# Kernel optimization log

Hardware: AMD Instinct MI355X
Metric: run time of the kernel (lower is better)

Reference implementation:

```python
import jax, jax.numpy as jnp
import numpy as np

N_NODES = 100000
N_EDGES = 1600000
D_IN = 128
D_OUT = 128


def setup_inputs() -> dict:
    key = jax.random.key(0)
    k1, k2, k3 = jax.random.split(key, 3)
    x = jax.random.normal(k1, (N_NODES, D_IN), dtype=jnp.float32)
    edge_index = jax.random.randint(k2, (2, N_EDGES), 0, N_NODES, dtype=jnp.int64)
    # glorot-style init for the lazily-created weight
    scale = jnp.sqrt(6.0 / (D_IN + D_OUT)).astype(jnp.float32)
    weight = jax.random.uniform(k3, (D_IN, D_OUT), dtype=jnp.float32, minval=-1.0, maxval=1.0) * scale
    bias = jnp.zeros((D_OUT,), dtype=jnp.float32)
    return {"x": x, "edge_index": edge_index, "weight": weight, "bias": bias}


def reference(x, edge_index, weight, bias):
    N = x.shape[0]
    row, col = edge_index[0], edge_index[1]
    # add_remaining_self_loops: drop existing self-loops (equivalently zero their
    # weight) and append a self-loop of weight 1.0 for every node (improved=False).
    ew = jnp.where(row == col, 0.0, 1.0).astype(x.dtype)
    loop = jnp.arange(N, dtype=row.dtype)
    row = jnp.concatenate([row, loop])
    col = jnp.concatenate([col, loop])
    ew = jnp.concatenate([ew, jnp.ones((N,), dtype=x.dtype)])
    # degree via scatter-add on destination (col), deg^{-1/2} with inf -> 0
    deg = jax.ops.segment_sum(ew, col, num_segments=N)
    deg_inv_sqrt = jnp.where(deg > 0, jax.lax.rsqrt(deg), 0.0).astype(x.dtype)
    norm = deg_inv_sqrt[row] * ew * deg_inv_sqrt[col]  # [E+N]
    # dense transform then gather-scale-scatter (GCN message passing, aggr='add')
    xw = x @ weight  # [N, D_OUT]
    msgs = norm[:, None] * xw[row]  # [E+N, D_OUT] gather on source nodes
    out = jax.ops.segment_sum(msgs, col, num_segments=N)  # scatter-add to dest
    return out + bias
```

## Files before the change

### kernel.cpp

```cpp
#include <hip/hip_runtime.h>
#include <hip/hip_bf16.h>

#define NN 100000
#define NE 1600000
#define D  128
#define NPAD 100352
#define NBLK 782
#define CAP  64

#define BSH    9
#define NB_C   196
#define CAPB   9216
#define PCHUNK 2048
#define PEPT   8
#define NPART  782

#define NSL    8
#define NGRP   3125
#define AGG_BLOCKS 2048

typedef __attribute__((ext_vector_type(8))) short short8;
typedef __attribute__((ext_vector_type(4))) float floatx4;
typedef __attribute__((ext_vector_type(2))) float fx2;
typedef __attribute__((ext_vector_type(4))) int intx4;

__device__ __forceinline__ unsigned short f2b(float f) {
    __hip_bfloat16 h = __float2bfloat16(f);
    return *(unsigned short*)&h;
}

__device__ __forceinline__ int swz(int row, int col_us) {
    return row * 128 + (col_us ^ ((row & 7) << 3));
}

__global__ __launch_bounds__(256) void k_part(const int* __restrict__ row,
                                              const int* __restrict__ col,
                                              int* __restrict__ bcnt,
                                              unsigned int* __restrict__ edgesP) {
    __shared__ int cur[NB_C], basep[NB_C];
    int t = threadIdx.x;
    size_t e0 = (size_t)blockIdx.x * PCHUNK;

    for (int i = t; i < NB_C; i += 256) cur[i] = 0;
    __syncthreads();

    unsigned int val[PEPT];
    int bk[PEPT], rk[PEPT];
#pragma unroll
    for (int i = 0; i < PEPT; ++i) {
        size_t e = e0 + i * 256 + t;
        bk[i] = -1;
        if (e < NE) {
            int r = row[e], c = col[e];
            if (r != c) {
                bk[i]  = c >> BSH;
                val[i] = (unsigned)r | ((unsigned)(c & 511) << 17);
                rk[i]  = atomicAdd(&cur[bk[i]], 1);
            }
        }
    }
    __syncthreads();

    for (int i = t; i < NB_C; i += 256)
        basep[i] = cur[i] ? atomicAdd(&bcnt[i], cur[i]) : 0;
    __syncthreads();

#pragma unroll
    for (int i = 0; i < PEPT; ++i) {
        if (bk[i] >= 0) {
            int pos = basep[bk[i]] + rk[i];
            if (pos < CAPB) edgesP[(size_t)bk[i] * CAPB + pos] = val[i];
        }
    }
}

__global__ __launch_bounds__(1024) void k_fine(const int* __restrict__ bcnt,
                                               const unsigned int* __restrict__ edgesP,
                                               int* __restrict__ counts,
                                               float* __restrict__ dinv,
                                               int* __restrict__ srcs) {
    __shared__ int cnt[512];
    int t = threadIdx.x, b = blockIdx.x;
    int n0 = b << BSH;
    for (int i = t; i < 512; i += 1024) cnt[i] = 0;
    __syncthreads();

    int m = min(bcnt[b], CAPB);
    const unsigned int* ep = edgesP + (size_t)b * CAPB;
    for (int i = t; i < m; i += 1024) {
        unsigned int v = ep[i];
        int c0 = v >> 17;
        int s  = v & 0x1FFFF;
        int pos = atomicAdd(&cnt[c0], 1);
        if (pos < CAP) srcs[(size_t)(n0 + c0) * CAP + pos] = s;
    }
    __syncthreads();
    for (int i = t; i < 512; i += 1024) {
        int n = n0 + i;
        int cv = cnt[i];
        counts[n] = min(cv, CAP);
        dinv[n] = rsqrtf((float)cv + 1.0f);
    }
}

__global__ void k_prep_w(const float* __restrict__ w, unsigned short* __restrict__ wt) {
    int i = blockIdx.x * 256 + threadIdx.x;
    int n = i >> 7, k = i & 127;
    wt[swz(n, k)] = f2b(w[k * D + n]);
}

__global__ __launch_bounds__(256, 2) void k_gemm_mfma(const float* __restrict__ x,
                                                      const unsigned short* __restrict__ wt,
                                                      const float* __restrict__ dinv,
                                                      unsigned short* __restrict__ yw) {
    __shared__ unsigned short sX[128 * 128];
    __shared__ unsigned short sW[128 * 128];
    __shared__ float sD[128];
    int tid = threadIdx.x;
    long row0 = (long)blockIdx.x * 128;

    if (tid < 128) {
        long gr = row0 + tid;
        sD[tid] = (gr < NN) ? dinv[gr] : 0.0f;
    }
    {
        const uint4* src = (const uint4*)wt;
        uint4* dst = (uint4*)sW;
#pragma unroll
        for (int j = 0; j < 8; ++j) dst[tid + j * 256] = src[tid + j * 256];
    }
#pragma unroll
    for (int j = 0; j < 16; ++j) {
        int i = tid + j * 256;
        int r = i >> 5, q = i & 31;
        floatx4 v = {0.f, 0.f, 0.f, 0.f};
        long gr = row0 + r;
        if (gr < NN) v = __builtin_nontemporal_load((const floatx4*)(x + gr * D + q * 4));
        ushort4 u;
        u.x = f2b(v.x); u.y = f2b(v.y); u.z = f2b(v.z); u.w = f2b(v.w);
        *(ushort4*)&sX[swz(r, q * 4)] = u;
    }
    __syncthreads();

    int lane = tid & 63, wave = tid >> 6;
    int wm = (wave & 1) * 64, wn = (wave >> 1) * 64;
    int lrow = lane & 15, lkb = (lane >> 4) * 8;

    floatx4 acc[4][4] = {};
#pragma unroll
    for (int kc = 0; kc < 4; ++kc) {
        int kb = kc * 32 + lkb;
        short8 bfr[4];
#pragma unroll
        for (int tn = 0; tn < 4; ++tn)
            bfr[tn] = *(const short8*)&sW[swz(wn + tn * 16 + lrow, kb)];
#pragma unroll
        for (int tm = 0; tm < 4; ++tm) {
            short8 afr = *(const short8*)&sX[swz(wm + tm * 16 + lrow, kb)];
#pragma unroll
            for (int tn = 0; tn < 4; ++tn)
                acc[tm][tn] = __builtin_amdgcn_mfma_f32_16x16x32_bf16(afr, bfr[tn], acc[tm][tn], 0, 0, 0);
        }
    }

    int orow = (lane >> 4) * 4;
    int ocol = lane & 15;
    int wb = wn >> 4;
#pragma unroll
    for (int tm = 0; tm < 4; ++tm) {
#pragma unroll
        for (int reg = 0; reg < 4; ++reg) {
            int  rt = wm + tm * 16 + orow + reg;
            long m  = row0 + rt;
            if (m < NN) {
                float dm = sD[rt];
                unsigned short* o = yw + ((size_t)wb * NN + m) * 16 + ocol;
#pragma unroll
                for (int tn = 0; tn < 4; ++tn)
                    o[(size_t)tn * NN * 16] = f2b(acc[tm][tn][reg] * dm);
            }
        }
    }
}

__global__ __launch_bounds__(256, 8) void k_agg(const int* __restrict__ counts,
                                                const int* __restrict__ srcs,
                                                const float* __restrict__ dinv,
                                                const unsigned int* __restrict__ ywd,
                                                const float* __restrict__ bias,
                                                float* __restrict__ out) {
    __shared__ int slds[32 * 40];
    int tid = threadIdx.x;
    int w = tid >> 6;
    int d = (tid >> 3) & 7;
    int j = tid & 7;
    int din = w * 8 + d;
    int sl = blockIdx.x & 7;

    const unsigned int* ywj = ywd + (size_t)sl * NN * 8 + j;
    fx2 b2 = *(const fx2*)(bias + sl * 16 + 2 * j);

    int r = tid >> 3, q = tid & 7;

    for (int grp = blockIdx.x >> 3; grp < NGRP; grp += AGG_BLOCKS / 8) {
        int c0 = grp * 32;
        {
            intx4 v = __builtin_nontemporal_load(
                (const intx4*)(srcs + (size_t)(c0 + r) * CAP + q * 4));
            *(intx4*)&slds[r * 40 + q * 4] = v;
        }
        __syncthreads();

        int c = c0 + din;
        int cnt = counts[c];
        float dc = dinv[c];
        const int* srow = slds + din * 40;

        unsigned int v0 = ywj[(size_t)c * 8];
        float a0 = __uint_as_float(v0 << 16);
        float a1 = __uint_as_float(v0 & 0xFFFF0000u);

        int lim = min(cnt, 32);
        int p = 0;
        for (; p + 4 <= lim; p += 4) {
            intx4 s4 = *(const intx4*)(srow + p);
            unsigned int g0 = ywj[(size_t)s4.x * 8];
            unsigned int g1 = ywj[(size_t)s4.y * 8];
            unsigned int g2 = ywj[(size_t)s4.z * 8];
            unsigned int g3 = ywj[(size_t)s4.w * 8];
            a0 += __uint_as_float(g0 << 16);  a1 += __uint_as_float(g0 & 0xFFFF0000u);
            a0 += __uint_as_float(g1 << 16);  a1 += __uint_as_float(g1 & 0xFFFF0000u);
            a0 += __uint_as_float(g2 << 16);  a1 += __uint_as_float(g2 & 0xFFFF0000u);
            a0 += __uint_as_float(g3 << 16);  a1 += __uint_as_float(g3 & 0xFFFF0000u);
        }
        for (; p < lim; ++p) {
            unsigned int g = ywj[(size_t)srow[p] * 8];
            a0 += __uint_as_float(g << 16);  a1 += __uint_as_float(g & 0xFFFF0000u);
        }
        if (cnt > 32) {
            const int* sp2 = srcs + (size_t)c * CAP;
            for (p = 32; p < cnt; ++p) {
                unsigned int g = ywj[(size_t)sp2[p] * 8];
                a0 += __uint_as_float(g << 16);  a1 += __uint_as_float(g & 0xFFFF0000u);
            }
        }

        fx2 o;
        o.x = dc * a0 + b2.x;
        o.y = dc * a1 + b2.y;
        __builtin_nontemporal_store(o, (fx2*)(out + (size_t)c * D + sl * 16 + 2 * j));
        __syncthreads();
    }
}

extern "C" void kernel_launch(void* const* d_in, const int* in_sizes, int n_in,
                              void* d_out, int out_size, void* d_ws, size_t ws_size,
                              hipStream_t stream) {
    const float* x    = (const float*)d_in[0];
    const int*   ei   = (const int*)d_in[1];
    const float* w    = (const float*)d_in[2];
    const float* bias = (const float*)d_in[3];
    float*       out  = (float*)d_out;

    const int* row = ei;
    const int* col = ei + NE;

    int*   counts = (int*)d_ws;
    float* dinv   = (float*)(counts + NPAD);
    int*   srcs   = (int*)(dinv + NPAD);
    unsigned short* yw = (unsigned short*)(srcs + (size_t)NN * CAP);
    unsigned short* wt = yw + (size_t)NN * D;
    int*   bcnt   = (int*)(wt + 128 * 128);
    unsigned int* edgesP = (unsigned int*)yw;

    hipMemsetAsync(bcnt, 0, NB_C * sizeof(int), stream);

    k_prep_w<<<64, 256, 0, stream>>>(w, wt);
    k_part<<<NPART, 256, 0, stream>>>(row, col, bcnt, edgesP);
    k_fine<<<NB_C, 1024, 0, stream>>>(bcnt, edgesP, counts, dinv, srcs);
    k_gemm_mfma<<<NBLK, 256, 0, stream>>>(x, wt, dinv, yw);
    k_agg<<<AGG_BLOCKS, 256, 0, stream>>>(counts, srcs, dinv, (const unsigned int*)yw, bias, out);
}
```

Baseline: 260.1 us.

## Process one destination per wave with shuffle-broadcast gathers and coalesced GEMM stores

The aggregation kernel now assigns one destination node per wavefront. Eight lane groups each gather a different source row's 16-column slice, and the partial sums are combined with cross-lane xor shuffles. This replaces the older layout of 32 destinations per block with an LDS staging buffer and block-wide barriers. The GEMM epilogue now stages its bf16 results through shared memory so that each row slice is written as contiguous 32-byte vector stores instead of scattered 2-byte stores. The new aggregation caps neighbours at 63 per node, and it wastes lanes on low-degree nodes because each wave handles a single destination.

```diff
diff --git a/kernel.cpp b/kernel.cpp
--- a/kernel.cpp
+++ b/kernel.cpp
@@ -15,14 +15,12 @@
 #define PEPT   8
 #define NPART  782
 
-#define NSL    8
-#define NGRP   3125
 #define AGG_BLOCKS 2048
+#define DESTS_PER_ROUND 1024
 
 typedef __attribute__((ext_vector_type(8))) short short8;
 typedef __attribute__((ext_vector_type(4))) float floatx4;
 typedef __attribute__((ext_vector_type(2))) float fx2;
-typedef __attribute__((ext_vector_type(4))) int intx4;
 
 __device__ __forceinline__ unsigned short f2b(float f) {
     __hip_bfloat16 h = __float2bfloat16(f);
@@ -163,22 +161,34 @@
         }
     }
 
+    __syncthreads();
+
     int orow = (lane >> 4) * 4;
     int ocol = lane & 15;
-    int wb = wn >> 4;
 #pragma unroll
     for (int tm = 0; tm < 4; ++tm) {
 #pragma unroll
         for (int reg = 0; reg < 4; ++reg) {
-            int  rt = wm + tm * 16 + orow + reg;
-            long m  = row0 + rt;
-            if (m < NN) {
-                float dm = sD[rt];
-                unsigned short* o = yw + ((size_t)wb * NN + m) * 16 + ocol;
-#pragma unroll
-                for (int tn = 0; tn < 4; ++tn)
-                    o[(size_t)tn * NN * 16] = f2b(acc[tm][tn][reg] * dm);
-            }
+            int rt = wm + tm * 16 + orow + reg;
+            float dm = sD[rt];
+#pragma unroll
+            for (int tn = 0; tn < 4; ++tn)
+                sX[swz(rt, wn + tn * 16 + ocol)] = f2b(acc[tm][tn][reg] * dm);
+        }
+    }
+    __syncthreads();
+
+#pragma unroll
+    for (int j = 0; j < 4; ++j) {
+        int i = tid + j * 256;
+        int r = i & 127, sl8 = i >> 7;
+        long gr = row0 + r;
+        if (gr < NN) {
+            uint4 v0 = *(const uint4*)&sX[swz(r, sl8 * 16)];
+            uint4 v1 = *(const uint4*)&sX[swz(r, sl8 * 16 + 8)];
+            unsigned short* dst = yw + ((size_t)sl8 * NN + gr) * 16;
+            *(uint4*)dst = v0;
+            *(uint4*)(dst + 8) = v1;
         }
     }
 }
@@ -189,67 +199,49 @@
                                                 const unsigned int* __restrict__ ywd,
                                                 const float* __restrict__ bias,
                                                 float* __restrict__ out) {
-    __shared__ int slds[32 * 40];
-    int tid = threadIdx.x;
-    int w = tid >> 6;
-    int d = (tid >> 3) & 7;
-    int j = tid & 7;
-    int din = w * 8 + d;
+    int lane = threadIdx.x & 63;
+    int wv = threadIdx.x >> 6;
     int sl = blockIdx.x & 7;
-
-    const unsigned int* ywj = ywd + (size_t)sl * NN * 8 + j;
+    int g = lane >> 3, j = lane & 7;
+
+    const unsigned int* yws = ywd + (size_t)sl * NN * 8 + j;
     fx2 b2 = *(const fx2*)(bias + sl * 16 + 2 * j);
 
-    int r = tid >> 3, q = tid & 7;
-
-    for (int grp = blockIdx.x >> 3; grp < NGRP; grp += AGG_BLOCKS / 8) {
-        int c0 = grp * 32;
-        {
-            intx4 v = __builtin_nontemporal_load(
-                (const intx4*)(srcs + (size_t)(c0 + r) * CAP + q * 4));
-            *(intx4*)&slds[r * 40 + q * 4] = v;
-        }
-        __syncthreads();
-
-        int c = c0 + din;
-        int cnt = counts[c];
-        float dc = dinv[c];
-        const int* srow = slds + din * 40;
-
-        unsigned int v0 = ywj[(size_t)c * 8];
-        float a0 = __uint_as_float(v0 << 16);
-        float a1 = __uint_as_float(v0 & 0xFFFF0000u);
-
-        int lim = min(cnt, 32);
-        int p = 0;
-        for (; p + 4 <= lim; p += 4) {
-            intx4 s4 = *(const intx4*)(srow + p);
-            unsigned int g0 = ywj[(size_t)s4.x * 8];
-            unsigned int g1 = ywj[(size_t)s4.y * 8];
-            unsigned int g2 = ywj[(size_t)s4.z * 8];
-            unsigned int g3 = ywj[(size_t)s4.w * 8];
-            a0 += __uint_as_float(g0 << 16);  a1 += __uint_as_float(g0 & 0xFFFF0000u);
-            a0 += __uint_as_float(g1 << 16);  a1 += __uint_as_float(g1 & 0xFFFF0000u);
-            a0 += __uint_as_float(g2 << 16);  a1 += __uint_as_float(g2 & 0xFFFF0000u);
-            a0 += __uint_as_float(g3 << 16);  a1 += __uint_as_float(g3 & 0xFFFF0000u);
-        }
-        for (; p < lim; ++p) {
-            unsigned int g = ywj[(size_t)srow[p] * 8];
-            a0 += __uint_as_float(g << 16);  a1 += __uint_as_float(g & 0xFFFF0000u);
-        }
-        if (cnt > 32) {
-            const int* sp2 = srcs + (size_t)c * CAP;
-            for (p = 32; p < cnt; ++p) {
-                unsigned int g = ywj[(size_t)sp2[p] * 8];
-                a0 += __uint_as_float(g << 16);  a1 += __uint_as_float(g & 0xFFFF0000u);
+    for (int c = (blockIdx.x >> 3) * 4 + wv; c < NN; c += DESTS_PER_ROUND) {
+        int cnt0 = min(counts[c], 63);
+        const int* sp = srcs + (size_t)c * CAP;
+        int mysrc = c;
+        if (lane >= 1 && lane <= cnt0) mysrc = sp[lane - 1];
+        int ec = cnt0 + 1;
+
+        float a0 = 0.0f, a1 = 0.0f;
+        for (int p = 0; p < ec; p += 16) {
+            int i0 = p + g, i1 = p + 8 + g;
+            int s0 = __shfl(mysrc, (i0 < ec) ? i0 : 0);
+            int s1 = __shfl(mysrc, (i1 < ec) ? i1 : 0);
+            unsigned int v0 = yws[(size_t)s0 * 8];
+            unsigned int v1 = yws[(size_t)s1 * 8];
+            if (i0 < ec) {
+                a0 += __uint_as_float(v0 << 16);
+                a1 += __uint_as_float(v0 & 0xFFFF0000u);
             }
-        }
-
-        fx2 o;
-        o.x = dc * a0 + b2.x;
-        o.y = dc * a1 + b2.y;
-        __builtin_nontemporal_store(o, (fx2*)(out + (size_t)c * D + sl * 16 + 2 * j));
-        __syncthreads();
+            if (i1 < ec) {
+                a0 += __uint_as_float(v1 << 16);
+                a1 += __uint_as_float(v1 & 0xFFFF0000u);
+            }
+        }
+
+        a0 += __shfl_xor(a0, 8);   a1 += __shfl_xor(a1, 8);
+        a0 += __shfl_xor(a0, 16);  a1 += __shfl_xor(a1, 16);
+        a0 += __shfl_xor(a0, 32);  a1 += __shfl_xor(a1, 32);
+
+        if (g == 0) {
+            float dc = dinv[c];
+            fx2 o;
+            o.x = dc * a0 + b2.x;
+            o.y = dc * a1 + b2.y;
+            __builtin_nontemporal_store(o, (fx2*)(out + (size_t)c * D + sl * 16 + 2 * j));
+        }
     }
 }
 
```

New measurement: 332.3 us. +27.8%, slower.
